# Optimization experiments

Hardware: AMD Instinct MI355X
Metric: run time of the kernel (lower is better)

## Reference

```python
import jax, jax.numpy as jnp
import numpy as np

N_USERS = 50000
N_ITEMS = 50000
E = 400000
S = 128   # in_feats_s (memory / GRU hidden)
T = 64    # in_feats_t (time encoding dim)
ED = 64   # edge feature dim
M = 2 * S + T + ED  # in_feats_m = 384

_BASIS_FREQ = jnp.asarray(1.0 / 10 ** np.linspace(0, 9, T), dtype=jnp.float32)


def time_encode(ts):
    # cos(ts * freq + phase), phase == 0
    return jnp.cos(ts[:, None] * _BASIS_FREQ[None, :])


def mean_message(src_mem, dst_mem, ts, e, src, dst, n_dst):
    # mail per edge: [E, 2S + T + ED]
    mail = jnp.concatenate(
        [src_mem[src], dst_mem[dst], time_encode(ts), e], axis=1)
    s = jax.ops.segment_sum(mail, dst, num_segments=n_dst)
    cnt = jax.ops.segment_sum(jnp.ones_like(ts), dst, num_segments=n_dst)
    return s / jnp.maximum(cnt, 1.0)[:, None]


def gru_step(x, h, w_ih, w_hh, b_ih, b_hh):
    # single-step PyTorch GRU; gate order r, z, n
    gi = x @ w_ih.T + b_ih
    gh = h @ w_hh.T + b_hh
    ir, iz, i_n = jnp.split(gi, 3, axis=1)
    hr, hz, h_n = jnp.split(gh, 3, axis=1)
    r = jax.nn.sigmoid(ir + hr)
    z = jax.nn.sigmoid(iz + hz)
    n = jnp.tanh(i_n + r * h_n)
    return (1.0 - z) * n + z * h


def setup_inputs() -> dict:
    key = jax.random.key(0)
    ks = jax.random.split(key, 16)
    sc = 1.0 / np.sqrt(S)
    return {
        "si":   jax.random.normal(ks[0], (N_USERS, S), jnp.float32),
        "sj":   jax.random.normal(ks[1], (N_ITEMS, S), jnp.float32),
        "si_r": jax.random.normal(ks[2], (N_ITEMS, S), jnp.float32),
        "sj_r": jax.random.normal(ks[3], (N_USERS, S), jnp.float32),
        "t":    jax.random.uniform(ks[4], (E,), jnp.float32),
        "t_r":  jax.random.uniform(ks[5], (E,), jnp.float32),
        "e":    jax.random.normal(ks[6], (E, ED), jnp.float32),
        "e_r":  jax.random.normal(ks[7], (E, ED), jnp.float32),
        "w_ih": jax.random.normal(ks[8], (3 * S, M), jnp.float32) * sc,
        "w_hh": jax.random.normal(ks[9], (3 * S, S), jnp.float32) * sc,
        "b_ih": jax.random.normal(ks[10], (3 * S,), jnp.float32) * sc,
        "b_hh": jax.random.normal(ks[11], (3 * S,), jnp.float32) * sc,
        "src_g":  jax.random.randint(ks[12], (E,), 0, N_USERS, jnp.int32),
        "dst_g":  jax.random.randint(ks[13], (E,), 0, N_ITEMS, jnp.int32),
        "src_gr": jax.random.randint(ks[14], (E,), 0, N_ITEMS, jnp.int32),
        "dst_gr": jax.random.randint(ks[15], (E,), 0, N_USERS, jnp.int32),
    }


def reference(si, sj, si_r, sj_r, t, t_r, e, e_r,
              w_ih, w_hh, b_ih, b_hh,
              src_g, dst_g, src_gr, dst_gr):
    # g: user -> item; g_r: item -> user
    mj = mean_message(si, sj, t, e, src_g, dst_g, N_ITEMS)       # messages to items
    mi = mean_message(si_r, sj_r, t_r, e_r, src_gr, dst_gr, N_USERS)  # messages to users
    si_out = gru_step(mi, sj_r, w_ih, w_hh, b_ih, b_hh)  # user memory update
    sj_out = gru_step(mj, sj, w_ih, w_hh, b_ih, b_hh)    # item memory update
    return (si_out, sj_out)
```

## Files before the change

### kernel.cpp

```cpp
#include <hip/hip_runtime.h>
#include <math.h>

#define NUSERS 50000
#define NITEMS 50000
#define NTOT   100000
#define NNODE  50000
#define NCHUNK 196
#define MTILES 6250
#define NMCHUNK 196
#define KDIM   512
#define NWAVES 8192

typedef __attribute__((ext_vector_type(4))) float f32x4;
typedef __attribute__((ext_vector_type(8))) short short8;
typedef unsigned int u32;

#define AS1 __attribute__((address_space(1)))
#define AS3 __attribute__((address_space(3)))

static __device__ __forceinline__ unsigned short f2bf(float f) {
  unsigned int u = __float_as_uint(f);
  u += 0x7fffu + ((u >> 16) & 1u);
  return (unsigned short)(u >> 16);
}

static __device__ __forceinline__ u32 pack2(float x, float y) {
  return (u32)f2bf(x) | ((u32)f2bf(y) << 16);
}

static __device__ __forceinline__ void gload_lds16(const void* g, void* l) {
  __builtin_amdgcn_global_load_lds((const AS1 u32*)g, (AS3 u32*)l, 16, 0, 0);
}

__global__ void pack_w_kernel(const float* __restrict__ w_ih,
                              const float* __restrict__ w_hh,
                              const float* __restrict__ b_ih,
                              const float* __restrict__ b_hh,
                              unsigned short* __restrict__ Wb,
                              float* __restrict__ bb) {
  int idx = blockIdx.x * 256 + threadIdx.x;
  int j = idx & 7, l = (idx >> 3) & 63, ktt = idx >> 9;
  int kt = ktt & 15, tt = ktt >> 4;
  int g = tt * 16 + (l & 15);
  int k = kt * 32 + (l >> 4) * 8 + j;
  float v;
  if (g < 256)      v = (k < 384) ? w_ih[g * 384 + k] : w_hh[g * 128 + (k - 384)];
  else if (g < 384) v = (k < 384) ? w_ih[g * 384 + k] : 0.0f;
  else              v = (k < 384) ? 0.0f : w_hh[(g - 128) * 128 + (k - 384)];
  Wb[idx] = f2bf(v);
  if (idx < 512) {
    float b = (idx < 256) ? (b_ih[idx] + b_hh[idx])
            : (idx < 384) ? b_ih[idx]
                          : b_hh[idx - 128];
    bb[idx] = b;
  }
}

__global__ void cast_mem_kernel(const float* __restrict__ si,
                                const float* __restrict__ si_r,
                                unsigned short* __restrict__ si_b,
                                unsigned short* __restrict__ sir_b) {
  int i = blockIdx.x * 256 + threadIdx.x;
  const float* src; unsigned short* dst; int off;
  if (i < 800000) { src = si;   dst = si_b;  off = i; }
  else            { src = si_r; dst = sir_b; off = i - 800000; }
  const f32x4* p = (const f32x4*)(src + (size_t)off * 8);
  f32x4 a = p[0], b = p[1];
  short8 o;
  o[0] = f2bf(a[0]); o[1] = f2bf(a[1]); o[2] = f2bf(a[2]); o[3] = f2bf(a[3]);
  o[4] = f2bf(b[0]); o[5] = f2bf(b[1]); o[6] = f2bf(b[2]); o[7] = f2bf(b[3]);
  *(short8*)(dst + (size_t)off * 8) = o;
}

__global__ void hist_kernel(const int* __restrict__ dst_g,
                            const int* __restrict__ dst_gr,
                            int* __restrict__ deg_j, int* __restrict__ deg_i, int E) {
  int i = blockIdx.x * 256 + threadIdx.x;
  if (i < E) atomicAdd(&deg_j[dst_g[i]], 1);
  else if (i < 2 * E) atomicAdd(&deg_i[dst_gr[i - E]], 1);
}

__global__ void chunksum_kernel(const int* __restrict__ deg_j,
                                const int* __restrict__ deg_i,
                                int* __restrict__ csum) {
  int c = blockIdx.x;
  const int* deg = (c < NCHUNK) ? deg_j : deg_i;
  int cc = (c < NCHUNK) ? c : c - NCHUNK;
  int t = threadIdx.x;
  int idx = cc * 256 + t;
  int v = (idx < NNODE) ? deg[idx] : 0;
  for (int off = 32; off; off >>= 1) v += __shfl_down(v, off, 64);
  __shared__ int wsum[4];
  if ((t & 63) == 0) wsum[t >> 6] = v;
  __syncthreads();
  if (t == 0) csum[c] = wsum[0] + wsum[1] + wsum[2] + wsum[3];
}

__global__ void chunkscan_kernel(const int* __restrict__ csum, int* __restrict__ coff) {
  int d = blockIdx.x;
  const int* cs = csum + d * NCHUNK;
  int* co = coff + d * NCHUNK;
  int t = threadIdx.x, lane = t & 63, w = t >> 6;
  int v = (t < NCHUNK) ? cs[t] : 0;
  int x = v;
  for (int off = 1; off < 64; off <<= 1) {
    int y = __shfl_up(x, off, 64);
    if (lane >= off) x += y;
  }
  __shared__ int wt[4];
  if (lane == 63) wt[w] = x;
  __syncthreads();
  int add = 0;
  for (int k = 0; k < 4; ++k) if (k < w) add += wt[k];
  if (t < NCHUNK) co[t] = add + x - v;
}

__global__ void localscan_kernel(const int* __restrict__ deg_j,
                                 const int* __restrict__ deg_i,
                                 const int* __restrict__ coff,
                                 int* __restrict__ rs_j, int* __restrict__ cur_j,
                                 int* __restrict__ rs_i, int* __restrict__ cur_i) {
  int c = blockIdx.x;
  bool dj = c < NCHUNK;
  const int* deg = dj ? deg_j : deg_i;
  int cc = dj ? c : c - NCHUNK;
  int* rs = dj ? rs_j : rs_i;
  int* cur = dj ? cur_j : cur_i;
  int base = coff[c];
  int t = threadIdx.x, lane = t & 63, w = t >> 6;
  int idx = cc * 256 + t;
  int v = (idx < NNODE) ? deg[idx] : 0;
  int x = v;
  for (int off = 1; off < 64; off <<= 1) {
    int y = __shfl_up(x, off, 64);
    if (lane >= off) x += y;
  }
  __shared__ int wt[4];
  if (lane == 63) wt[w] = x;
  __syncthreads();
  int add = 0;
  for (int k = 0; k < 4; ++k) if (k < w) add += wt[k];
  int ex = base + add + x - v;
  if (idx < NNODE) { rs[idx] = ex; cur[idx] = ex; }
}

__global__ void fill_kernel(const int* __restrict__ src_g, const int* __restrict__ dst_g,
                            const float* __restrict__ t,
                            const int* __restrict__ src_gr, const int* __restrict__ dst_gr,
                            const float* __restrict__ t_r,
                            int* __restrict__ cur_j, int* __restrict__ cur_i,
                            int4* __restrict__ recP_j, int4* __restrict__ recP_i,
                            int E) {
  int i = blockIdx.x * 256 + threadIdx.x;
  if (i < E) {
    int pos = atomicAdd(&cur_j[dst_g[i]], 1);
    recP_j[pos] = make_int4(src_g[i], i, __float_as_int(t[i]), 0);
  } else if (i < 2 * E) {
    int k = i - E;
    int pos = atomicAdd(&cur_i[dst_gr[k]], 1);
    recP_i[pos] = make_int4(src_gr[k], k, __float_as_int(t_r[k]), 0);
  }
}

__global__ __launch_bounds__(256) void gather_kernel(
    const unsigned short* __restrict__ si_b, const unsigned short* __restrict__ sir_b,
    const float* __restrict__ sj, const float* __restrict__ sj_r,
    const float* __restrict__ e, const float* __restrict__ e_r,
    const int* __restrict__ rs_j, const int* __restrict__ rs_i,
    const int* __restrict__ deg_j, const int* __restrict__ deg_i,
    const int4* __restrict__ recP_j, const int4* __restrict__ recP_i,
    unsigned short* __restrict__ Xb) {
  __shared__ __align__(16) unsigned short rowbuf[4][512];
  int wid = threadIdx.x >> 6, lane = threadIdx.x & 63;
  int gwave = blockIdx.x * 4 + wid;
  float freq = __expf((float)lane * -0.3289407276f);
  unsigned short* rb = rowbuf[wid];
  u32* rb32 = (u32*)rb;

  for (int node = gwave; node < NTOT; node += NWAVES) {
    bool user = node < NUSERS;
    int idx = user ? node : node - NUSERS;
    const unsigned short* smem = user ? sir_b : si_b;
    const float* h  = user ? sj_r : sj;
    const float* ef = user ? e_r : e;
    int start = __builtin_amdgcn_readfirstlane((user ? rs_i : rs_j)[idx]);
    int deg   = __builtin_amdgcn_readfirstlane((user ? deg_i : deg_j)[idx]);
    const int4* rec = user ? recP_i : recP_j;

    float2 hvf = *(const float2*)(h + (size_t)idx * 128 + 2 * lane);

    float asx = 0.f, asy = 0.f;
    float at  = 0.f;
    float ae  = 0.f;

    for (int base = 0; base < deg; base += 64) {
      int nn = deg - base; if (nn > 64) nn = 64;
      int cl = (lane < nn) ? base + lane : base + nn - 1;
      int4 r = rec[start + cl];
      int full = nn & ~7;
      for (int j0 = 0; j0 < full; j0 += 8) {
        int s0 = __builtin_amdgcn_readlane(r.x, j0 + 0), e0 = __builtin_amdgcn_readlane(r.y, j0 + 0);
        int s1 = __builtin_amdgcn_readlane(r.x, j0 + 1), e1 = __builtin_amdgcn_readlane(r.y, j0 + 1);
        int s2 = __builtin_amdgcn_readlane(r.x, j0 + 2), e2 = __builtin_amdgcn_readlane(r.y, j0 + 2);
        int s3 = __builtin_amdgcn_readlane(r.x, j0 + 3), e3 = __builtin_amdgcn_readlane(r.y, j0 + 3);
        int s4 = __builtin_amdgcn_readlane(r.x, j0 + 4), e4 = __builtin_amdgcn_readlane(r.y, j0 + 4);
        int s5 = __builtin_amdgcn_readlane(r.x, j0 + 5), e5 = __builtin_amdgcn_readlane(r.y, j0 + 5);
        int s6 = __builtin_amdgcn_readlane(r.x, j0 + 6), e6 = __builtin_amdgcn_readlane(r.y, j0 + 6);
        int s7 = __builtin_amdgcn_readlane(r.x, j0 + 7), e7 = __builtin_amdgcn_readlane(r.y, j0 + 7);

        u32 v0 = *(const u32*)(smem + ((size_t)s0 << 7) + 2 * lane);
        u32 v1 = *(const u32*)(smem + ((size_t)s1 << 7) + 2 * lane);
        u32 v2 = *(const u32*)(smem + ((size_t)s2 << 7) + 2 * lane);
        u32 v3 = *(const u32*)(smem + ((size_t)s3 << 7) + 2 * lane);
        u32 v4 = *(const u32*)(smem + ((size_t)s4 << 7) + 2 * lane);
        u32 v5 = *(const u32*)(smem + ((size_t)s5 << 7) + 2 * lane);
        u32 v6 = *(const u32*)(smem + ((size_t)s6 << 7) + 2 * lane);
        u32 v7 = *(const u32*)(smem + ((size_t)s7 << 7) + 2 * lane);
        float f0 = ef[((size_t)e0 << 6) + lane];
        float f1 = ef[((size_t)e1 << 6) + lane];
        float f2 = ef[((size_t)e2 << 6) + lane];
        float f3 = ef[((size_t)e3 << 6) + lane];
        float f4 = ef[((size_t)e4 << 6) + lane];
        float f5 = ef[((size_t)e5 << 6) + lane];
        float f6 = ef[((size_t)e6 << 6) + lane];
        float f7 = ef[((size_t)e7 << 6) + lane];

        float c0 = __cosf(__int_as_float(__builtin_amdgcn_readlane(r.z, j0 + 0)) * freq);
        float c1 = __cosf(__int_as_float(__builtin_amdgcn_readlane(r.z, j0 + 1)) * freq);
        float c2 = __cosf(__int_as_float(__builtin_amdgcn_readlane(r.z, j0 + 2)) * freq);
        float c3 = __cosf(__int_as_float(__builtin_amdgcn_readlane(r.z, j0 + 3)) * freq);
        float c4 = __cosf(__int_as_float(__builtin_amdgcn_readlane(r.z, j0 + 4)) * freq);
        float c5 = __cosf(__int_as_float(__builtin_amdgcn_readlane(r.z, j0 + 5)) * freq);
        float c6 = __cosf(__int_as_float(__builtin_amdgcn_readlane(r.z, j0 + 6)) * freq);
        float c7 = __cosf(__int_as_float(__builtin_amdgcn_readlane(r.z, j0 + 7)) * freq);

        float l0 = __uint_as_float(v0 << 16), g0 = __uint_as_float(v0 & 0xffff0000u);
        float l1 = __uint_as_float(v1 << 16), g1 = __uint_as_float(v1 & 0xffff0000u);
        float l2 = __uint_as_float(v2 << 16), g2 = __uint_as_float(v2 & 0xffff0000u);
        float l3 = __uint_as_float(v3 << 16), g3 = __uint_as_float(v3 & 0xffff0000u);
        float l4 = __uint_as_float(v4 << 16), g4 = __uint_as_float(v4 & 0xffff0000u);
        float l5 = __uint_as_float(v5 << 16), g5 = __uint_as_float(v5 & 0xffff0000u);
        float l6 = __uint_as_float(v6 << 16), g6 = __uint_as_float(v6 & 0xffff0000u);
        float l7 = __uint_as_float(v7 << 16), g7 = __uint_as_float(v7 & 0xffff0000u);

        asx += ((l0 + l1) + (l2 + l3)) + ((l4 + l5) + (l6 + l7));
        asy += ((g0 + g1) + (g2 + g3)) + ((g4 + g5) + (g6 + g7));
        at  += ((c0 + c1) + (c2 + c3)) + ((c4 + c5) + (c6 + c7));
        ae  += ((f0 + f1) + (f2 + f3)) + ((f4 + f5) + (f6 + f7));
      }
      if (full < nn) {
        int j0 = full;
        int j1 = (j0 + 1 < nn) ? j0 + 1 : nn - 1;
        int j2 = (j0 + 2 < nn) ? j0 + 2 : nn - 1;
        int j3 = (j0 + 3 < nn) ? j0 + 3 : nn - 1;
        int j4 = (j0 + 4 < nn) ? j0 + 4 : nn - 1;
        int j5 = (j0 + 5 < nn) ? j0 + 5 : nn - 1;
        int j6 = (j0 + 6 < nn) ? j0 + 6 : nn - 1;
        float w1 = (j0 + 1 < nn) ? 1.0f : 0.0f;
        float w2 = (j0 + 2 < nn) ? 1.0f : 0.0f;
        float w3 = (j0 + 3 < nn) ? 1.0f : 0.0f;
        float w4 = (j0 + 4 < nn) ? 1.0f : 0.0f;
        float w5 = (j0 + 5 < nn) ? 1.0f : 0.0f;
        float w6 = (j0 + 6 < nn) ? 1.0f : 0.0f;

        int s0 = __builtin_amdgcn_readlane(r.x, j0), e0 = __builtin_amdgcn_readlane(r.y, j0);
        int s1 = __builtin_amdgcn_readlane(r.x, j1), e1 = __builtin_amdgcn_readlane(r.y, j1);
        int s2 = __builtin_amdgcn_readlane(r.x, j2), e2 = __builtin_amdgcn_readlane(r.y, j2);
        int s3 = __builtin_amdgcn_readlane(r.x, j3), e3 = __builtin_amdgcn_readlane(r.y, j3);
        int s4 = __builtin_amdgcn_readlane(r.x, j4), e4 = __builtin_amdgcn_readlane(r.y, j4);
        int s5 = __builtin_amdgcn_readlane(r.x, j5), e5 = __builtin_amdgcn_readlane(r.y, j5);
        int s6 = __builtin_amdgcn_readlane(r.x, j6), e6 = __builtin_amdgcn_readlane(r.y, j6);

        u32 v0 = *(const u32*)(smem + ((size_t)s0 << 7) + 2 * lane);
        u32 v1 = *(const u32*)(smem + ((size_t)s1 << 7) + 2 * lane);
        u32 v2 = *(const u32*)(smem + ((size_t)s2 << 7) + 2 * lane);
        u32 v3 = *(const u32*)(smem + ((size_t)s3 << 7) + 2 * lane);
        u32 v4 = *(const u32*)(smem + ((size_t)s4 << 7) + 2 * lane);
        u32 v5 = *(const u32*)(smem + ((size_t)s5 << 7) + 2 * lane);
        u32 v6 = *(const u32*)(smem + ((size_t)s6 << 7) + 2 * lane);
        float f0 = ef[((size_t)e0 << 6) + lane];
        float f1 = ef[((size_t)e1 << 6) + lane];
        float f2 = ef[((size_t)e2 << 6) + lane];
        float f3 = ef[((size_t)e3 << 6) + lane];
        float f4 = ef[((size_t)e4 << 6) + lane];
        float f5 = ef[((size_t)e5 << 6) + lane];
        float f6 = ef[((size_t)e6 << 6) + lane];

        float c0 = __cosf(__int_as_float(__builtin_amdgcn_readlane(r.z, j0)) * freq);
        float c1 = __cosf(__int_as_float(__builtin_amdgcn_readlane(r.z, j1)) * freq);
        float c2 = __cosf(__int_as_float(__builtin_amdgcn_readlane(r.z, j2)) * freq);
        float c3 = __cosf(__int_as_float(__builtin_amdgcn_readlane(r.z, j3)) * freq);
        float c4 = __cosf(__int_as_float(__builtin_amdgcn_readlane(r.z, j4)) * freq);
        float c5 = __cosf(__int_as_float(__builtin_amdgcn_readlane(r.z, j5)) * freq);
        float c6 = __cosf(__int_as_float(__builtin_amdgcn_readlane(r.z, j6)) * freq);

        float l0 = __uint_as_float(v0 << 16), g0 = __uint_as_float(v0 & 0xffff0000u);
        float l1 = __uint_as_float(v1 << 16), g1 = __uint_as_float(v1 & 0xffff0000u);
        float l2 = __uint_as_float(v2 << 16), g2 = __uint_as_float(v2 & 0xffff0000u);
        float l3 = __uint_as_float(v3 << 16), g3 = __uint_as_float(v3 & 0xffff0000u);
        float l4 = __uint_as_float(v4 << 16), g4 = __uint_as_float(v4 & 0xffff0000u);
        float l5 = __uint_as_float(v5 << 16), g5 = __uint_as_float(v5 & 0xffff0000u);
        float l6 = __uint_as_float(v6 << 16), g6 = __uint_as_float(v6 & 0xffff0000u);

        asx += l0 + w1 * l1 + w2 * l2 + w3 * l3 + w4 * l4 + w5 * l5 + w6 * l6;
        asy += g0 + w1 * g1 + w2 * g2 + w3 * g3 + w4 * g4 + w5 * g5 + w6 * g6;
        at  += c0 + w1 * c1 + w2 * c2 + w3 * c3 + w4 * c4 + w5 * c5 + w6 * c6;
        ae  += f0 + w1 * f1 + w2 * f2 + w3 * f3 + w4 * f4 + w5 * f5 + w6 * f6;
      }
    }

    float invc = (deg > 0) ? 1.0f / (float)deg : 0.0f;
    float hz   = (deg > 0) ? 1.0f : 0.0f;

    rb32[lane]       = pack2(asx * invc, asy * invc);
    rb32[64 + lane]  = pack2(hvf.x * hz, hvf.y * hz);
    rb[256 + lane]   = f2bf(at * invc);
    rb[320 + lane]   = f2bf(ae * invc);
    rb32[192 + lane] = pack2(hvf.x, hvf.y);

    short8 vv = *(const short8*)(rb + lane * 8);
    *(short8*)(Xb + (size_t)node * 512 + lane * 8) = vv;
  }
}

__global__ __launch_bounds__(512, 2) void gemm_gru_kernel(
    const unsigned short* __restrict__ Xb,
    const unsigned short* __restrict__ Wb,
    const float* __restrict__ bb,
    const float* __restrict__ sj_r,
    const float* __restrict__ sj,
    float* __restrict__ out) {
  __shared__ __align__(16) unsigned short sW[65536];
  int wid = threadIdx.x >> 6, lane = threadIdx.x & 63;
  int jp = blockIdx.x & 3;
  int mcbase = (blockIdx.x >> 2) * 32;
  int col16 = lane & 15, quad = lane >> 4;

  {
    int g = wid >> 1, p = wid & 1;
    int tt = g * 8 + jp * 2 + p;
    const unsigned short* wp = Wb + ((size_t)tt * 16 * 64 + lane) * 8;
#pragma unroll
    for (int kt = 0; kt < 16; ++kt)
      gload_lds16(wp + (size_t)kt * 512, sW + (wid * 16 + kt) * 512);
  }
  __syncthreads();

  int mt[4];
  const unsigned short* Ap[4];
#pragma unroll
  for (int mi = 0; mi < 4; ++mi) {
    mt[mi] = mcbase + wid * 4 + mi;
    int mc = (mt[mi] < MTILES) ? mt[mi] : MTILES - 1;
    Ap[mi] = Xb + (size_t)(mc * 16 + col16) * 512 + quad * 8;
  }

  f32x4 acc[4][8];
#pragma unroll
  for (int mi = 0; mi < 4; ++mi)
#pragma unroll
    for (int t8 = 0; t8 < 8; ++t8) acc[mi][t8] = (f32x4)0.0f;

  for (int kt = 0; kt < 16; ++kt) {
    short8 a[4];
#pragma unroll
    for (int mi = 0; mi < 4; ++mi)
      a[mi] = *(const short8*)(Ap[mi] + kt * 32);
    short8 b[8];
#pragma unroll
    for (int t8 = 0; t8 < 8; ++t8)
      b[t8] = *(const short8*)(sW + (t8 * 16 + kt) * 512 + lane * 8);
#pragma unroll
    for (int mi = 0; mi < 4; ++mi)
#pragma unroll
      for (int t8 = 0; t8 < 8; ++t8)
        acc[mi][t8] = __builtin_amdgcn_mfma_f32_16x16x32_bf16(a[mi], b[t8], acc[mi][t8], 0, 0, 0);
  }

#pragma unroll
  for (int p = 0; p < 2; ++p) {
    int cc = (jp * 2 + p) * 16 + col16;
    float bbr = bb[cc], bbz = bb[128 + cc], bbn = bb[256 + cc], bbh = bb[384 + cc];
#pragma unroll
    for (int mi = 0; mi < 4; ++mi) {
      if (mt[mi] >= MTILES) continue;
#pragma unroll
      for (int r = 0; r < 4; ++r) {
        int row = mt[mi] * 16 + quad * 4 + r;
        float rp  = acc[mi][0 + p][r] + bbr;
        float zp  = acc[mi][2 + p][r] + bbz;
        float inp = acc[mi][4 + p][r] + bbn;
        float hnp = acc[mi][6 + p][r] + bbh;
        float rg = 1.0f / (1.0f + __expf(-rp));
        float zg = 1.0f / (1.0f + __expf(-zp));
        float ng = tanhf(inp + rg * hnp);
        float hv = (row < NUSERS) ? sj_r[(size_t)row * 128 + cc]
                                  : sj[(size_t)(row - NUSERS) * 128 + cc];
        out[(size_t)row * 128 + cc] = (1.0f - zg) * ng + zg * hv;
      }
    }
  }
}

extern "C" void kernel_launch(void* const* d_in, const int* in_sizes, int n_in,
                              void* d_out, int out_size, void* d_ws, size_t ws_size,
                              hipStream_t stream) {
  const float* si   = (const float*)d_in[0];
  const float* sj   = (const float*)d_in[1];
  const float* si_r = (const float*)d_in[2];
  const float* sj_r = (const float*)d_in[3];
  const float* t    = (const float*)d_in[4];
  const float* t_r  = (const float*)d_in[5];
  const float* e    = (const float*)d_in[6];
  const float* e_r  = (const float*)d_in[7];
  const float* w_ih = (const float*)d_in[8];
  const float* w_hh = (const float*)d_in[9];
  const float* b_ih = (const float*)d_in[10];
  const float* b_hh = (const float*)d_in[11];
  const int* src_g  = (const int*)d_in[12];
  const int* dst_g  = (const int*)d_in[13];
  const int* src_gr = (const int*)d_in[14];
  const int* dst_gr = (const int*)d_in[15];
  int E = in_sizes[4];

  unsigned short* Xb = (unsigned short*)d_ws;
  unsigned short* Wb = Xb + (size_t)NTOT * 512;
  float* bb   = (float*)(Wb + 262144);
  int* deg_j  = (int*)(bb + 512);
  int* deg_i  = deg_j + NNODE;
  int* rs_j   = deg_i + NNODE;
  int* rs_i   = rs_j + NNODE;
  int* cur_j  = rs_i + NNODE;
  int* cur_i  = cur_j + NNODE;
  int* csum   = cur_i + NNODE;
  int* coff   = csum + 2 * NCHUNK;
  int4* recP_j = (int4*)(coff + 2 * NCHUNK);
  int4* recP_i = recP_j + E;
  unsigned short* si_b  = (unsigned short*)(recP_i + E);
  unsigned short* sir_b = si_b + 6400000;

  hipMemsetAsync(deg_j, 0, 2 * NNODE * sizeof(int), stream);

  pack_w_kernel<<<(512 * 512) / 256, 256, 0, stream>>>(w_ih, w_hh, b_ih, b_hh, Wb, bb);
  cast_mem_kernel<<<6250, 256, 0, stream>>>(si, si_r, si_b, sir_b);

  int blks2E = (2 * E + 255) / 256;
  hist_kernel<<<blks2E, 256, 0, stream>>>(dst_g, dst_gr, deg_j, deg_i, E);
  chunksum_kernel<<<2 * NCHUNK, 256, 0, stream>>>(deg_j, deg_i, csum);
  chunkscan_kernel<<<2, 256, 0, stream>>>(csum, coff);
  localscan_kernel<<<2 * NCHUNK, 256, 0, stream>>>(deg_j, deg_i, coff, rs_j, cur_j, rs_i, cur_i);
  fill_kernel<<<blks2E, 256, 0, stream>>>(src_g, dst_g, t, src_gr, dst_gr, t_r,
                                          cur_j, cur_i, recP_j, recP_i, E);

  gather_kernel<<<NWAVES / 4, 256, 0, stream>>>(si_b, sir_b, sj, sj_r, e, e_r,
                                                rs_j, rs_i, deg_j, deg_i,
                                                recP_j, recP_i, Xb);

  float* out = (float*)d_out;
  gemm_gru_kernel<<<NMCHUNK * 4, 512, 0, stream>>>(Xb, Wb, bb, sj_r, sj, out);
}
```

Before: 622.9 us.

## Restructure GRU GEMM to stream weights from global and share A rows across waves

The GEMM+GRU kernel no longer stages a 128KB weight slice in LDS. Each block now covers 4 M-tiles, and each of the 8 waves owns one 16-column group across all 4 gates, reading B fragments straight from global memory (L2-resident). All waves in a block load the same A rows, so the X matrix is read once instead of four times across column-split blocks. This removes the LDS preload and barrier and raises the occupancy target to 3 blocks. The cost is redundant A loads across waves within a block, B traffic through L1/L2 on every k-step, and many more, smaller blocks.

```diff
diff --git a/kernel.cpp b/kernel.cpp
--- a/kernel.cpp
+++ b/kernel.cpp
@@ -7,7 +7,6 @@
 #define NNODE  50000
 #define NCHUNK 196
 #define MTILES 6250
-#define NMCHUNK 196
 #define KDIM   512
 #define NWAVES 8192
 
@@ -323,81 +322,68 @@
   }
 }
 
-__global__ __launch_bounds__(512, 2) void gemm_gru_kernel(
+__global__ __launch_bounds__(512, 3) void gemm_gru_kernel(
     const unsigned short* __restrict__ Xb,
     const unsigned short* __restrict__ Wb,
     const float* __restrict__ bb,
     const float* __restrict__ sj_r,
     const float* __restrict__ sj,
     float* __restrict__ out) {
-  __shared__ __align__(16) unsigned short sW[65536];
   int wid = threadIdx.x >> 6, lane = threadIdx.x & 63;
-  int jp = blockIdx.x & 3;
-  int mcbase = (blockIdx.x >> 2) * 32;
+  int mbase = blockIdx.x * 4;
   int col16 = lane & 15, quad = lane >> 4;
 
-  {
-    int g = wid >> 1, p = wid & 1;
-    int tt = g * 8 + jp * 2 + p;
-    const unsigned short* wp = Wb + ((size_t)tt * 16 * 64 + lane) * 8;
-#pragma unroll
-    for (int kt = 0; kt < 16; ++kt)
-      gload_lds16(wp + (size_t)kt * 512, sW + (wid * 16 + kt) * 512);
-  }
-  __syncthreads();
+  f32x4 acc[4][4];
+#pragma unroll
+  for (int mi = 0; mi < 4; ++mi)
+#pragma unroll
+    for (int g = 0; g < 4; ++g) acc[mi][g] = (f32x4)0.0f;
 
   int mt[4];
   const unsigned short* Ap[4];
 #pragma unroll
   for (int mi = 0; mi < 4; ++mi) {
-    mt[mi] = mcbase + wid * 4 + mi;
+    mt[mi] = mbase + mi;
     int mc = (mt[mi] < MTILES) ? mt[mi] : MTILES - 1;
     Ap[mi] = Xb + (size_t)(mc * 16 + col16) * 512 + quad * 8;
   }
-
-  f32x4 acc[4][8];
-#pragma unroll
-  for (int mi = 0; mi < 4; ++mi)
-#pragma unroll
-    for (int t8 = 0; t8 < 8; ++t8) acc[mi][t8] = (f32x4)0.0f;
-
+  const unsigned short* Bp[4];
+#pragma unroll
+  for (int g = 0; g < 4; ++g)
+    Bp[g] = Wb + ((size_t)(g * 8 + wid) * 16 * 64 + lane) * 8;
+
+#pragma unroll
   for (int kt = 0; kt < 16; ++kt) {
-    short8 a[4];
+    short8 a[4], b[4];
+#pragma unroll
+    for (int mi = 0; mi < 4; ++mi) a[mi] = *(const short8*)(Ap[mi] + kt * 32);
+#pragma unroll
+    for (int g = 0; g < 4; ++g)    b[g]  = *(const short8*)(Bp[g] + (size_t)kt * 512);
 #pragma unroll
     for (int mi = 0; mi < 4; ++mi)
-      a[mi] = *(const short8*)(Ap[mi] + kt * 32);
-    short8 b[8];
-#pragma unroll
-    for (int t8 = 0; t8 < 8; ++t8)
-      b[t8] = *(const short8*)(sW + (t8 * 16 + kt) * 512 + lane * 8);
-#pragma unroll
-    for (int mi = 0; mi < 4; ++mi)
-#pragma unroll
-      for (int t8 = 0; t8 < 8; ++t8)
-        acc[mi][t8] = __builtin_amdgcn_mfma_f32_16x16x32_bf16(a[mi], b[t8], acc[mi][t8], 0, 0, 0);
-  }
-
-#pragma unroll
-  for (int p = 0; p < 2; ++p) {
-    int cc = (jp * 2 + p) * 16 + col16;
-    float bbr = bb[cc], bbz = bb[128 + cc], bbn = bb[256 + cc], bbh = bb[384 + cc];
-#pragma unroll
-    for (int mi = 0; mi < 4; ++mi) {
-      if (mt[mi] >= MTILES) continue;
-#pragma unroll
-      for (int r = 0; r < 4; ++r) {
-        int row = mt[mi] * 16 + quad * 4 + r;
-        float rp  = acc[mi][0 + p][r] + bbr;
-        float zp  = acc[mi][2 + p][r] + bbz;
-        float inp = acc[mi][4 + p][r] + bbn;
-        float hnp = acc[mi][6 + p][r] + bbh;
-        float rg = 1.0f / (1.0f + __expf(-rp));
-        float zg = 1.0f / (1.0f + __expf(-zp));
-        float ng = tanhf(inp + rg * hnp);
-        float hv = (row < NUSERS) ? sj_r[(size_t)row * 128 + cc]
-                                  : sj[(size_t)(row - NUSERS) * 128 + cc];
-        out[(size_t)row * 128 + cc] = (1.0f - zg) * ng + zg * hv;
-      }
+#pragma unroll
+      for (int g = 0; g < 4; ++g)
+        acc[mi][g] = __builtin_amdgcn_mfma_f32_16x16x32_bf16(a[mi], b[g], acc[mi][g], 0, 0, 0);
+  }
+
+  int cc = wid * 16 + col16;
+  float bbr = bb[cc], bbz = bb[128 + cc], bbn = bb[256 + cc], bbh = bb[384 + cc];
+#pragma unroll
+  for (int mi = 0; mi < 4; ++mi) {
+    if (mt[mi] >= MTILES) continue;
+#pragma unroll
+    for (int r = 0; r < 4; ++r) {
+      int row = mt[mi] * 16 + quad * 4 + r;
+      float rp  = acc[mi][0][r] + bbr;
+      float zp  = acc[mi][1][r] + bbz;
+      float inp = acc[mi][2][r] + bbn;
+      float hnp = acc[mi][3][r] + bbh;
+      float rg = 1.0f / (1.0f + __expf(-rp));
+      float zg = 1.0f / (1.0f + __expf(-zp));
+      float ng = tanhf(inp + rg * hnp);
+      float hv = (row < NUSERS) ? sj_r[(size_t)row * 128 + cc]
+                                : sj[(size_t)(row - NUSERS) * 128 + cc];
+      out[(size_t)row * 128 + cc] = (1.0f - zg) * ng + zg * hv;
     }
   }
 }
@@ -457,5 +443,5 @@
                                                 recP_j, recP_i, Xb);
 
   float* out = (float*)d_out;
-  gemm_gru_kernel<<<NMCHUNK * 4, 512, 0, stream>>>(Xb, Wb, bb, sj_r, sj, out);
-}
+  gemm_gru_kernel<<<(MTILES + 3) / 4, 512, 0, stream>>>(Xb, Wb, bb, sj_r, sj, out);
+}
```

New measurement: 653.1 us. 1.05x slower.
